# Kernel optimization log

Measured on AMD Instinct MI355X. Metric: run time of the kernel, lower is better.

## Reference

```python
import jax, jax.numpy as jnp
import numpy as np

B, N, IN, OUT = 8, 2048, 128, 128


def setup_inputs() -> dict:
    key = jax.random.key(0)
    k1, k2 = jax.random.split(key)
    inputs = jax.random.normal(k1, (B, N, IN), dtype=jnp.float32)
    # TruncatedNormal(stddev=1/sqrt(fan_in)) approximated by scaled normal
    w = jax.random.normal(k2, (IN, OUT), dtype=jnp.float32) / np.sqrt(IN).astype(np.float32)
    return {"inputs": inputs, "w": w}


def reference(inputs, w):
    # inputs: [B, N, IN]; w: [IN, OUT]
    # tropical linear: logsumexp over the contracted (input) axis of the
    # broadcast outer-sum inputs[..., :, None] + w[None, None, :, :]
    scores = inputs[..., :, None] + w[None, None, :, :]  # [B, N, IN, OUT]
    return jax.scipy.special.logsumexp(scores, axis=2)    # [B, N, OUT]
```

## Files before the change

kernel.cpp:

```cpp
#include <hip/hip_runtime.h>
#include <hip/hip_bf16.h>


using bf16x8 = __attribute__((ext_vector_type(8))) short;
using f32x4  = __attribute__((ext_vector_type(4))) float;

__device__ __forceinline__ unsigned short f2bf(float v) {
    __hip_bfloat16 b = __float2bfloat16(v);
    return __builtin_bit_cast(unsigned short, b);
}

__global__ __launch_bounds__(1024) void trop_kernel(const float* __restrict__ x,
                                                    const float* __restrict__ w,
                                                    float* __restrict__ out) {
    __shared__ uint4 ewl[2048];

    const int tid  = threadIdx.x;
    const int lane = tid & 63;
    const int wv   = tid >> 6;
    const int R    = wv >> 2;
    const int Cs   = wv & 3;
    const int r16  = lane & 15;
    const int g    = lane >> 4;

    const int r0   = blockIdx.x * 64 + R * 16;
    const int grow = r0 + r16;

    const float* xp = x + (size_t)grow * 128 + g * 8;
    float4 xv[8];
#pragma unroll
    for (int kb = 0; kb < 4; ++kb) {
#pragma unroll
        for (int h = 0; h < 2; ++h)
            xv[kb * 2 + h] = *reinterpret_cast<const float4*>(xp + kb * 32 + h * 4);
    }

#pragma unroll
    for (int r = 0; r < 2; ++r) {
        int s  = r * 1024 + tid;
        int f  = s >> 6;
        int L  = s & 63;
        int kb = f & 3;
        int c  = f >> 2;
        int o  = c * 16 + (L & 15);
        const float* wp = w + (size_t)(kb * 32 + (L >> 4) * 8) * 128 + o;
        unsigned int pk[4];
#pragma unroll
        for (int e = 0; e < 4; ++e) {
            unsigned short lo = f2bf(__expf(wp[(2 * e)     * 128]));
            unsigned short hi = f2bf(__expf(wp[(2 * e + 1) * 128]));
            pk[e] = (unsigned int)lo | ((unsigned int)hi << 16);
        }
        ewl[f * 64 + L] = make_uint4(pk[0], pk[1], pk[2], pk[3]);
    }

    bf16x8 afrag[4];
#pragma unroll
    for (int kb = 0; kb < 4; ++kb) {
#pragma unroll
        for (int h = 0; h < 2; ++h) {
            float4 v = xv[kb * 2 + h];
            afrag[kb][h * 4 + 0] = (short)f2bf(__expf(v.x));
            afrag[kb][h * 4 + 1] = (short)f2bf(__expf(v.y));
            afrag[kb][h * 4 + 2] = (short)f2bf(__expf(v.z));
            afrag[kb][h * 4 + 3] = (short)f2bf(__expf(v.w));
        }
    }

    __syncthreads();

    f32x4 acc[2] = {};
#pragma unroll
    for (int kb = 0; kb < 4; ++kb) {
#pragma unroll
        for (int cc = 0; cc < 2; ++cc) {
            int f = (Cs * 2 + cc) * 4 + kb;
            bf16x8 b = *reinterpret_cast<const bf16x8*>(&ewl[f * 64 + lane]);
            acc[cc] = __builtin_amdgcn_mfma_f32_16x16x32_bf16(afrag[kb], b, acc[cc], 0, 0, 0);
        }
    }

#pragma unroll
    for (int cc = 0; cc < 2; ++cc) {
        int col = Cs * 32 + cc * 16 + r16;
        float* op = out + (size_t)(r0 + g * 4) * 128 + col;
#pragma unroll
        for (int q = 0; q < 4; ++q)
            op[(size_t)q * 128] = __logf(acc[cc][q]);
    }
}

extern "C" void kernel_launch(void* const* d_in, const int* in_sizes, int n_in,
                              void* d_out, int out_size, void* d_ws, size_t ws_size,
                              hipStream_t stream) {
    const float* x = (const float*)d_in[0];
    const float* w = (const float*)d_in[1];
    float* out = (float*)d_out;
    trop_kernel<<<256, 1024, 0, stream>>>(x, w, out);
}
```

Baseline: 12.61 us.

## Split exp(w) preparation into separate kernel and read B fragments from global

Moves the per-block exp/bf16 packing of the weight matrix into a small prep kernel that writes a 32KB pre-swizzled buffer to workspace once per call. The main kernel drops LDS staging and the block barrier, reads B fragments straight from global/L2, and uses smaller 256-thread blocks over 1024 blocks of 16 rows each. This removes the redundant 256x recomputation of exp(w) and the sync, at the cost of an extra kernel launch, and each block now reads the full weight buffer through cache.

```diff
diff --git a/kernel.cpp b/kernel.cpp
--- a/kernel.cpp
+++ b/kernel.cpp
@@ -10,20 +10,34 @@
     return __builtin_bit_cast(unsigned short, b);
 }
 
-__global__ __launch_bounds__(1024) void trop_kernel(const float* __restrict__ x,
-                                                    const float* __restrict__ w,
-                                                    float* __restrict__ out) {
-    __shared__ uint4 ewl[2048];
+__global__ __launch_bounds__(64) void prep_kernel(const float* __restrict__ w,
+                                                  uint4* __restrict__ ws) {
+    const int f  = blockIdx.x;
+    const int L  = threadIdx.x;
+    const int kb = f & 3;
+    const int c  = f >> 2;
+    const int o  = c * 16 + (L & 15);
+    const float* wp = w + (size_t)(kb * 32 + (L >> 4) * 8) * 128 + o;
+    unsigned int pk[4];
+#pragma unroll
+    for (int e = 0; e < 4; ++e) {
+        unsigned short lo = f2bf(__expf(wp[(2 * e)     * 128]));
+        unsigned short hi = f2bf(__expf(wp[(2 * e + 1) * 128]));
+        pk[e] = (unsigned int)lo | ((unsigned int)hi << 16);
+    }
+    ws[f * 64 + L] = make_uint4(pk[0], pk[1], pk[2], pk[3]);
+}
 
+__global__ __launch_bounds__(256) void main_kernel(const float* __restrict__ x,
+                                                   const uint4* __restrict__ ws,
+                                                   float* __restrict__ out) {
     const int tid  = threadIdx.x;
     const int lane = tid & 63;
     const int wv   = tid >> 6;
-    const int R    = wv >> 2;
-    const int Cs   = wv & 3;
     const int r16  = lane & 15;
     const int g    = lane >> 4;
 
-    const int r0   = blockIdx.x * 64 + R * 16;
+    const int r0   = blockIdx.x * 16;
     const int grow = r0 + r16;
 
     const float* xp = x + (size_t)grow * 128 + g * 8;
@@ -33,25 +47,6 @@
 #pragma unroll
         for (int h = 0; h < 2; ++h)
             xv[kb * 2 + h] = *reinterpret_cast<const float4*>(xp + kb * 32 + h * 4);
-    }
-
-#pragma unroll
-    for (int r = 0; r < 2; ++r) {
-        int s  = r * 1024 + tid;
-        int f  = s >> 6;
-        int L  = s & 63;
-        int kb = f & 3;
-        int c  = f >> 2;
-        int o  = c * 16 + (L & 15);
-        const float* wp = w + (size_t)(kb * 32 + (L >> 4) * 8) * 128 + o;
-        unsigned int pk[4];
-#pragma unroll
-        for (int e = 0; e < 4; ++e) {
-            unsigned short lo = f2bf(__expf(wp[(2 * e)     * 128]));
-            unsigned short hi = f2bf(__expf(wp[(2 * e + 1) * 128]));
-            pk[e] = (unsigned int)lo | ((unsigned int)hi << 16);
-        }
-        ewl[f * 64 + L] = make_uint4(pk[0], pk[1], pk[2], pk[3]);
     }
 
     bf16x8 afrag[4];
@@ -67,22 +62,20 @@
         }
     }
 
-    __syncthreads();
-
     f32x4 acc[2] = {};
 #pragma unroll
     for (int kb = 0; kb < 4; ++kb) {
 #pragma unroll
         for (int cc = 0; cc < 2; ++cc) {
-            int f = (Cs * 2 + cc) * 4 + kb;
-            bf16x8 b = *reinterpret_cast<const bf16x8*>(&ewl[f * 64 + lane]);
+            int f = (wv * 2 + cc) * 4 + kb;
+            bf16x8 b = *reinterpret_cast<const bf16x8*>(&ws[f * 64 + lane]);
             acc[cc] = __builtin_amdgcn_mfma_f32_16x16x32_bf16(afrag[kb], b, acc[cc], 0, 0, 0);
         }
     }
 
 #pragma unroll
     for (int cc = 0; cc < 2; ++cc) {
-        int col = Cs * 32 + cc * 16 + r16;
+        int col = wv * 32 + cc * 16 + r16;
         float* op = out + (size_t)(r0 + g * 4) * 128 + col;
 #pragma unroll
         for (int q = 0; q < 4; ++q)
@@ -96,5 +89,8 @@
     const float* x = (const float*)d_in[0];
     const float* w = (const float*)d_in[1];
     float* out = (float*)d_out;
-    trop_kernel<<<256, 1024, 0, stream>>>(x, w, out);
+    uint4* ws = (uint4*)d_ws;
+
+    prep_kernel<<<32, 64, 0, stream>>>(w, ws);
+    main_kernel<<<1024, 256, 0, stream>>>(x, ws, out);
 }
```

After: 17.07 us. 1.35x slower.
